# Kernel tuning notes

Hardware: AMD Instinct MI355X
Metric: run time of the kernel (lower is better)

## Reference

```python
import jax, jax.numpy as jnp
import numpy as np

B, S, HID = 4, 1024, 2048
H, D = 16, 128
CACHE_LEN = 2048


def setup_inputs() -> dict:
    key = jax.random.key(0)
    ks = jax.random.split(key, 5)
    return {
        "x": jax.random.normal(ks[0], (B, S, HID), jnp.float32),
        "cached_k": jax.random.normal(ks[1], (CACHE_LEN, H, D), jnp.float32),
        "cached_v": jax.random.normal(ks[2], (CACHE_LEN, H, D), jnp.float32),
        "w_qkv": jax.random.normal(ks[3], (3 * HID, HID), jnp.float32) * 0.02,
        "b_qkv": jnp.zeros((3 * HID,), jnp.float32),
        "w_proj": jax.random.normal(ks[4], (HID, HID), jnp.float32) * 0.02,
        "b_proj": jnp.zeros((HID,), jnp.float32),
    }


def reference(x, cached_k, cached_v, w_qkv, b_qkv, w_proj, b_proj):
    b, s, hid = x.shape
    h, d = H, D
    # fused QKV projection (nn.Linear uses y = x @ W.T + b)
    qkv = x @ w_qkv.T + b_qkv                      # [B,S,3*HID]
    q, k, v = jnp.split(qkv, 3, axis=-1)
    q = q.reshape(b, s, h, d).transpose(0, 2, 1, 3)  # [B,H,S,D]
    k = k.reshape(b, s, h, d).transpose(0, 2, 1, 3)
    v = v.reshape(b, s, h, d).transpose(0, 2, 1, 3)
    # cached KV: [cache_len,H,D] -> [H,cache_len,D] -> broadcast over batch
    clen = cached_k.shape[0]
    ck = jnp.broadcast_to(cached_k.transpose(1, 0, 2)[None], (b, h, clen, d))
    cv = jnp.broadcast_to(cached_v.transpose(1, 0, 2)[None], (b, h, clen, d))
    k = jnp.concatenate([ck, k], axis=2)           # [B,H,clen+S,D]
    v = jnp.concatenate([cv, v], axis=2)
    # non-causal scaled dot-product attention
    scale = 1.0 / jnp.sqrt(jnp.asarray(d, x.dtype))
    scores = jnp.einsum('bhqd,bhkd->bhqk', q, k) * scale
    attn = jax.nn.softmax(scores, axis=-1)
    out = jnp.einsum('bhqk,bhkd->bhqd', attn, v)   # [B,H,S,D]
    out = out.transpose(0, 2, 1, 3).reshape(b, s, hid)
    return out @ w_proj.T + b_proj
```

## Files before the change

### kernel.cpp

```cpp
#include <hip/hip_runtime.h>
#include <cstdint>
#include <cstddef>

typedef _Float16 f16;
typedef _Float16 f16x4 __attribute__((ext_vector_type(4)));
typedef _Float16 f16x8 __attribute__((ext_vector_type(8)));
typedef float f32x4 __attribute__((ext_vector_type(4)));

__device__ __forceinline__ void gld_lds16(const void* gp, void* lp) {
  __builtin_amdgcn_global_load_lds(
      (__attribute__((address_space(1))) void*)(void*)gp,
      (__attribute__((address_space(3))) void*)lp, 16, 0, 0);
}

__global__ __launch_bounds__(256) void cast_plain(const float* __restrict__ in,
                                                  f16* __restrict__ out, int n4) {
  int i = blockIdx.x * 256 + threadIdx.x;
  if (i >= n4) return;
  float4 v = ((const float4*)in)[i];
  f16x4 o = {(f16)v.x, (f16)v.y, (f16)v.z, (f16)v.w};
  ((f16x4*)out)[i] = o;
}

__global__ __launch_bounds__(256) void cast_ck(const float* __restrict__ in,
                                               f16* __restrict__ out) {
  int i = blockIdx.x * 256 + threadIdx.x;
  int d4 = i & 31, hh = (i >> 5) & 15, l = i >> 9;
  float4 v = ((const float4*)in)[((size_t)l * 16 + hh) * 32 + d4];
  f16x4 o = {(f16)v.x, (f16)v.y, (f16)v.z, (f16)v.w};
  ((f16x4*)out)[((size_t)hh * 2048 + l) * 32 + d4] = o;
}

__global__ __launch_bounds__(256) void cast_cvt(const float* __restrict__ in,
                                                f16* __restrict__ out) {
  __shared__ float tl[32][129];
  int hh = blockIdx.x & 15;
  int l0 = (blockIdx.x >> 4) * 32;
  int t = threadIdx.x;
#pragma unroll
  for (int j = 0; j < 4; j++) {
    int idx = j * 256 + t;
    int l = idx >> 5, d4 = idx & 31;
    float4 v = ((const float4*)in)[(((size_t)(l0 + l)) * 16 + hh) * 32 + d4];
    tl[l][d4 * 4 + 0] = v.x;
    tl[l][d4 * 4 + 1] = v.y;
    tl[l][d4 * 4 + 2] = v.z;
    tl[l][d4 * 4 + 3] = v.w;
  }
  __syncthreads();
#pragma unroll
  for (int j = 0; j < 4; j++) {
    int idx = j * 256 + t;
    int d = idx >> 3, l4 = (idx & 7) * 4;
    f16x4 o = {(f16)tl[l4 + 0][d], (f16)tl[l4 + 1][d],
               (f16)tl[l4 + 2][d], (f16)tl[l4 + 3][d]};
    ((f16x4*)(out + ((size_t)hh * 128 + d) * 2048 + l0))[l4 >> 2] = o;
  }
}

template <int EPI>
__global__ __launch_bounds__(256, 2) void gemm_bt(
    const f16* __restrict__ A, const f16* __restrict__ Bm,
    const float* __restrict__ bias, float* __restrict__ Cf, int M, int N, int K,
    f16* __restrict__ qb, f16* __restrict__ knb, f16* __restrict__ vtnb) {
  __shared__ f16 Al[128 * 32];
  __shared__ f16 Bl[128 * 32];
  const int t = threadIdx.x;
  const int lane = t & 63;
  const int w = t >> 6;
  const int bm = blockIdx.x * 128;
  const int bn = blockIdx.y * 128;
  const int wr = w >> 1, wc = w & 1;

  f32x4 acc[4][4] = {};

  const int srow = lane >> 2;
  const int soff = (lane & 3) * 8;
  const int colr = lane & 15;
  const int k0 = (lane >> 4) * 8;

  const int nk = K >> 5;
  for (int kt = 0; kt < nk; kt++) {
#pragma unroll
    for (int j = 0; j < 2; j++) {
      int c = j * 4 + w;
      int r = c * 16 + srow;
      gld_lds16(A + (size_t)(bm + r) * K + (size_t)kt * 32 + soff,
                (char*)Al + c * 1024);
      gld_lds16(Bm + (size_t)(bn + r) * K + (size_t)kt * 32 + soff,
                (char*)Bl + c * 1024);
    }
    __syncthreads();
    f16x8 af[4], bg[4];
#pragma unroll
    for (int mi = 0; mi < 4; mi++)
      af[mi] = *(const f16x8*)&Al[(wr * 64 + mi * 16 + colr) * 32 + k0];
#pragma unroll
    for (int ni = 0; ni < 4; ni++)
      bg[ni] = *(const f16x8*)&Bl[(wc * 64 + ni * 16 + colr) * 32 + k0];
#pragma unroll
    for (int mi = 0; mi < 4; mi++)
#pragma unroll
      for (int ni = 0; ni < 4; ni++)
        acc[mi][ni] = __builtin_amdgcn_mfma_f32_16x16x32_f16(
            af[mi], bg[ni], acc[mi][ni], 0, 0, 0);
    __syncthreads();
  }

  const float scale = 0.08838834764831845f;
#pragma unroll
  for (int mi = 0; mi < 4; mi++) {
#pragma unroll
    for (int ni = 0; ni < 4; ni++) {
      int n = bn + wc * 64 + ni * 16 + colr;
      int m0 = bm + wr * 64 + mi * 16 + ((lane >> 4) << 2);
      float bv = bias[n];
      f32x4 v = acc[mi][ni];
#pragma unroll
      for (int j = 0; j < 4; j++) {
        int m = m0 + j;
        float val = v[j] + bv;
        if (EPI == 0) {
          int bb = m >> 10, s = m & 1023;
          if (n < 2048) {
            int hh = n >> 7, d = n & 127;
            qb[(((size_t)(bb * 16 + hh)) * 1024 + s) * 128 + d] =
                (f16)(val * scale);
          } else if (n < 4096) {
            int n2 = n - 2048, hh = n2 >> 7, d = n2 & 127;
            knb[(((size_t)(bb * 16 + hh)) * 1024 + s) * 128 + d] = (f16)val;
          } else {
            int n2 = n - 4096, hh = n2 >> 7, d = n2 & 127;
            vtnb[((size_t)(bb * 16 + hh) * 128 + d) * 1024 + s] = (f16)val;
          }
        } else {
          Cf[(size_t)m * N + n] = val;
        }
      }
    }
  }
}

__global__ __launch_bounds__(256, 2) void attn_fwd(
    const f16* __restrict__ qb, const f16* __restrict__ knb,
    const f16* __restrict__ vtnb, const f16* __restrict__ ckb,
    const f16* __restrict__ cvtb, f16* __restrict__ attb) {
  __shared__ f16 Kl[64 * 128];
  __shared__ f16 Vl[128 * 64];
  __shared__ f16 Pl[4][32 * 64];
  const int t = threadIdx.x;
  const int lane = t & 63;
  const int w = t >> 6;
  const int qblk = blockIdx.x;
  const int bh = blockIdx.y;
  const int hh = bh & 15;
  const int colr = lane & 15;
  const int k0 = (lane >> 4) * 8;
  const int qbase = qblk * 128 + w * 32;

  f16x8 qf[2][4];
#pragma unroll
  for (int mi = 0; mi < 2; mi++) {
    const f16* Qp = qb + ((size_t)bh * 1024 + qbase + mi * 16 + colr) * 128 + k0;
#pragma unroll
    for (int c = 0; c < 4; c++) qf[mi][c] = *(const f16x8*)(Qp + c * 32);
  }

  float lrun[2][4];
  f32x4 o[2][8];
#pragma unroll
  for (int mi = 0; mi < 2; mi++) {
#pragma unroll
    for (int j = 0; j < 4; j++) lrun[mi][j] = 0.f;
#pragma unroll
    for (int dt = 0; dt < 8; dt++) o[mi][dt] = {0.f, 0.f, 0.f, 0.f};
  }

  const int srowK = lane >> 4;
  const int soffK = (lane & 15) * 8;
  const int srowV = lane >> 3;
  const int soffV = (lane & 7) * 8;
  f16* pw = &Pl[w][0];

  for (int kt = 0; kt < 48; kt++) {
    const int l0 = kt * 64;
    const f16* ks;
    const f16* vs;
    int vstride;
    if (l0 < 2048) {
      ks = ckb + ((size_t)hh * 2048 + l0) * 128;
      vs = cvtb + (size_t)hh * 128 * 2048 + l0;
      vstride = 2048;
    } else {
      ks = knb + ((size_t)bh * 1024 + (l0 - 2048)) * 128;
      vs = vtnb + (size_t)bh * 128 * 1024 + (l0 - 2048);
      vstride = 1024;
    }
#pragma unroll
    for (int j = 0; j < 4; j++) {
      int c = j * 4 + w;
      gld_lds16(ks + (size_t)(c * 4 + srowK) * 128 + soffK, (char*)Kl + c * 1024);
      gld_lds16(vs + (size_t)(c * 8 + srowV) * (size_t)vstride + soffV,
                (char*)Vl + c * 1024);
    }
    __syncthreads();

    f32x4 sc[2][4];
#pragma unroll
    for (int ct = 0; ct < 4; ct++) {
      f16x8 kf[4];
#pragma unroll
      for (int c = 0; c < 4; c++)
        kf[c] = *(const f16x8*)&Kl[(ct * 16 + colr) * 128 + c * 32 + k0];
#pragma unroll
      for (int mi = 0; mi < 2; mi++) {
        f32x4 a = {0.f, 0.f, 0.f, 0.f};
#pragma unroll
        for (int c = 0; c < 4; c++)
          a = __builtin_amdgcn_mfma_f32_16x16x32_f16(qf[mi][c], kf[c], a, 0, 0, 0);
        sc[mi][ct] = a;
      }
    }

#pragma unroll
    for (int mi = 0; mi < 2; mi++) {
#pragma unroll
      for (int j = 0; j < 4; j++) {
        int r = (lane >> 4) * 4 + j;
        float acc = 0.f;
#pragma unroll
        for (int ct = 0; ct < 4; ct++) {
          float p = __expf(sc[mi][ct][j]);
          acc += p;
          pw[(mi * 16 + r) * 64 + ct * 16 + colr] = (f16)p;
        }
        lrun[mi][j] += acc;
      }
    }

    f16x8 pa[2][2];
#pragma unroll
    for (int mi = 0; mi < 2; mi++)
#pragma unroll
      for (int ksl = 0; ksl < 2; ksl++)
        pa[mi][ksl] = *(const f16x8*)&pw[(mi * 16 + colr) * 64 + ksl * 32 + k0];
#pragma unroll
    for (int dt = 0; dt < 8; dt++) {
      f16x8 vf0 = *(const f16x8*)&Vl[(dt * 16 + colr) * 64 + k0];
      f16x8 vf1 = *(const f16x8*)&Vl[(dt * 16 + colr) * 64 + 32 + k0];
#pragma unroll
      for (int mi = 0; mi < 2; mi++) {
        o[mi][dt] = __builtin_amdgcn_mfma_f32_16x16x32_f16(pa[mi][0], vf0,
                                                           o[mi][dt], 0, 0, 0);
        o[mi][dt] = __builtin_amdgcn_mfma_f32_16x16x32_f16(pa[mi][1], vf1,
                                                           o[mi][dt], 0, 0, 0);
      }
    }
    __syncthreads();
  }

  const int bb = bh >> 4;
#pragma unroll
  for (int mi = 0; mi < 2; mi++) {
    float rinv[4];
#pragma unroll
    for (int j = 0; j < 4; j++) {
      float s = lrun[mi][j];
#pragma unroll
      for (int sh = 1; sh < 16; sh <<= 1) s += __shfl_xor(s, sh, 64);
      rinv[j] = 1.0f / s;
    }
#pragma unroll
    for (int dt = 0; dt < 8; dt++) {
#pragma unroll
      for (int j = 0; j < 4; j++) {
        int r = (lane >> 4) * 4 + j;
        int m = bb * 1024 + qblk * 128 + w * 32 + mi * 16 + r;
        int n = hh * 128 + dt * 16 + colr;
        attb[(size_t)m * 2048 + n] = (f16)(o[mi][dt][j] * rinv[j]);
      }
    }
  }
}

extern "C" void kernel_launch(void* const* d_in, const int* in_sizes, int n_in,
                              void* d_out, int out_size, void* d_ws,
                              size_t ws_size, hipStream_t stream) {
  const float* x = (const float*)d_in[0];
  const float* ck = (const float*)d_in[1];
  const float* cv = (const float*)d_in[2];
  const float* wqkv = (const float*)d_in[3];
  const float* bqkv = (const float*)d_in[4];
  const float* wproj = (const float*)d_in[5];
  const float* bproj = (const float*)d_in[6];
  float* out = (float*)d_out;

  char* ws = (char*)d_ws;
  size_t off = 0;
  auto alloc = [&](size_t bytes) {
    char* p = ws + off;
    off += bytes;
    return p;
  };
  f16* xb = (f16*)alloc(4096ull * 2048 * 2);
  f16* wqb = (f16*)alloc(6144ull * 2048 * 2);
  f16* wpb = (f16*)alloc(2048ull * 2048 * 2);
  f16* ckb = (f16*)alloc(16ull * 2048 * 128 * 2);
  f16* cvtb = (f16*)alloc(16ull * 128 * 2048 * 2);
  f16* qb = (f16*)alloc(64ull * 1024 * 128 * 2);
  f16* knb = (f16*)alloc(64ull * 1024 * 128 * 2);
  f16* vtnb = (f16*)alloc(64ull * 128 * 1024 * 2);
  f16* attb = xb;
  (void)ws_size;

  cast_plain<<<8192, 256, 0, stream>>>(x, xb, 2097152);
  cast_plain<<<12288, 256, 0, stream>>>(wqkv, wqb, 3145728);
  cast_plain<<<4096, 256, 0, stream>>>(wproj, wpb, 1048576);
  cast_ck<<<4096, 256, 0, stream>>>(ck, ckb);
  cast_cvt<<<1024, 256, 0, stream>>>(cv, cvtb);

  gemm_bt<0><<<dim3(32, 48), 256, 0, stream>>>(xb, wqb, bqkv, nullptr, 4096,
                                               6144, 2048, qb, knb, vtnb);
  attn_fwd<<<dim3(8, 64), 256, 0, stream>>>(qb, knb, vtnb, ckb, cvtb, attb);
  gemm_bt<1><<<dim3(32, 16), 256, 0, stream>>>(attb, wpb, bproj, out, 4096,
                                               2048, 2048, nullptr, nullptr,
                                               nullptr);
}
```

Baseline: 542.1 us.

## Double-buffer LDS tiles in GEMM and attention, XOR-swizzle attention LDS

Both the projection GEMM and the attention kernel now use two LDS buffers. The next K/V (or A/B) tile is issued with global_load_lds while MFMAs run on the current tile, which hides global load latency behind compute. The attention kernel also XOR-swizzles K, V and the per-wave P tile on both the write and read side to remove LDS bank conflicts caused by the power-of-two row strides. The cost is higher LDS use: attention goes to about 80KB per block, which may limit occupancy to two blocks per CU.

```diff
diff --git a/kernel.cpp b/kernel.cpp
--- a/kernel.cpp
+++ b/kernel.cpp
@@ -1,6 +1,7 @@
 #include <hip/hip_runtime.h>
 #include <cstdint>
 #include <cstddef>
+#include <type_traits>
 
 typedef _Float16 f16;
 typedef _Float16 f16x4 __attribute__((ext_vector_type(4)));
@@ -63,8 +64,8 @@
     const f16* __restrict__ A, const f16* __restrict__ Bm,
     const float* __restrict__ bias, float* __restrict__ Cf, int M, int N, int K,
     f16* __restrict__ qb, f16* __restrict__ knb, f16* __restrict__ vtnb) {
-  __shared__ f16 Al[128 * 32];
-  __shared__ f16 Bl[128 * 32];
+  __shared__ f16 Al[2][128 * 32];
+  __shared__ f16 Bl[2][128 * 32];
   const int t = threadIdx.x;
   const int lane = t & 63;
   const int w = t >> 6;
@@ -78,32 +79,47 @@
   const int soff = (lane & 3) * 8;
   const int colr = lane & 15;
   const int k0 = (lane >> 4) * 8;
-
   const int nk = K >> 5;
-  for (int kt = 0; kt < nk; kt++) {
+
+  auto stage = [&](int kt, auto bufc) {
+    constexpr int buf = decltype(bufc)::value;
 #pragma unroll
     for (int j = 0; j < 2; j++) {
       int c = j * 4 + w;
       int r = c * 16 + srow;
       gld_lds16(A + (size_t)(bm + r) * K + (size_t)kt * 32 + soff,
-                (char*)Al + c * 1024);
+                (char*)&Al[buf][0] + c * 1024);
       gld_lds16(Bm + (size_t)(bn + r) * K + (size_t)kt * 32 + soff,
-                (char*)Bl + c * 1024);
-    }
-    __syncthreads();
+                (char*)&Bl[buf][0] + c * 1024);
+    }
+  };
+  auto tile = [&](auto bufc) {
+    constexpr int buf = decltype(bufc)::value;
     f16x8 af[4], bg[4];
 #pragma unroll
     for (int mi = 0; mi < 4; mi++)
-      af[mi] = *(const f16x8*)&Al[(wr * 64 + mi * 16 + colr) * 32 + k0];
+      af[mi] = *(const f16x8*)&Al[buf][(wr * 64 + mi * 16 + colr) * 32 + k0];
 #pragma unroll
     for (int ni = 0; ni < 4; ni++)
-      bg[ni] = *(const f16x8*)&Bl[(wc * 64 + ni * 16 + colr) * 32 + k0];
+      bg[ni] = *(const f16x8*)&Bl[buf][(wc * 64 + ni * 16 + colr) * 32 + k0];
 #pragma unroll
     for (int mi = 0; mi < 4; mi++)
 #pragma unroll
       for (int ni = 0; ni < 4; ni++)
         acc[mi][ni] = __builtin_amdgcn_mfma_f32_16x16x32_f16(
             af[mi], bg[ni], acc[mi][ni], 0, 0, 0);
+  };
+  std::integral_constant<int, 0> B0;
+  std::integral_constant<int, 1> B1;
+
+  stage(0, B0);
+  __syncthreads();
+  for (int kt = 0; kt < nk; kt += 2) {
+    stage(kt + 1, B1);
+    tile(B0);
+    __syncthreads();
+    if (kt + 2 < nk) stage(kt + 2, B0);
+    tile(B1);
     __syncthreads();
   }
 
@@ -145,8 +161,8 @@
     const f16* __restrict__ qb, const f16* __restrict__ knb,
     const f16* __restrict__ vtnb, const f16* __restrict__ ckb,
     const f16* __restrict__ cvtb, f16* __restrict__ attb) {
-  __shared__ f16 Kl[64 * 128];
-  __shared__ f16 Vl[128 * 64];
+  __shared__ f16 Kl[2][64 * 128];
+  __shared__ f16 Vl[2][128 * 64];
   __shared__ f16 Pl[4][32 * 64];
   const int t = threadIdx.x;
   const int lane = t & 63;
@@ -155,7 +171,8 @@
   const int bh = blockIdx.y;
   const int hh = bh & 15;
   const int colr = lane & 15;
-  const int k0 = (lane >> 4) * 8;
+  const int g = lane >> 4;
+  const int k0 = g * 8;
   const int qbase = qblk * 128 + w * 32;
 
   f16x8 qf[2][4];
@@ -176,13 +193,12 @@
     for (int dt = 0; dt < 8; dt++) o[mi][dt] = {0.f, 0.f, 0.f, 0.f};
   }
 
-  const int srowK = lane >> 4;
-  const int soffK = (lane & 15) * 8;
-  const int srowV = lane >> 3;
-  const int soffV = (lane & 7) * 8;
+  const int csK_l = lane & 15;
+  const int csV_l = lane & 7;
   f16* pw = &Pl[w][0];
 
-  for (int kt = 0; kt < 48; kt++) {
+  auto stage = [&](int kt, auto bufc) {
+    constexpr int buf = decltype(bufc)::value;
     const int l0 = kt * 64;
     const f16* ks;
     const f16* vs;
@@ -199,19 +215,25 @@
 #pragma unroll
     for (int j = 0; j < 4; j++) {
       int c = j * 4 + w;
-      gld_lds16(ks + (size_t)(c * 4 + srowK) * 128 + soffK, (char*)Kl + c * 1024);
-      gld_lds16(vs + (size_t)(c * 8 + srowV) * (size_t)vstride + soffV,
-                (char*)Vl + c * 1024);
-    }
-    __syncthreads();
-
+      int rowK = c * 4 + g;
+      gld_lds16(ks + (size_t)rowK * 128 + ((csK_l ^ (rowK & 7)) * 8),
+                (char*)&Kl[buf][0] + c * 1024);
+      int rowV = c * 8 + (lane >> 3);
+      gld_lds16(vs + (size_t)rowV * (size_t)vstride + ((csV_l ^ (rowV & 7)) * 8),
+                (char*)&Vl[buf][0] + c * 1024);
+    }
+  };
+
+  auto tile = [&](auto bufc) {
+    constexpr int buf = decltype(bufc)::value;
     f32x4 sc[2][4];
 #pragma unroll
     for (int ct = 0; ct < 4; ct++) {
       f16x8 kf[4];
 #pragma unroll
       for (int c = 0; c < 4; c++)
-        kf[c] = *(const f16x8*)&Kl[(ct * 16 + colr) * 128 + c * 32 + k0];
+        kf[c] = *(const f16x8*)&Kl[buf][(ct * 16 + colr) * 128 +
+                                        ((c * 32 + k0) ^ ((colr & 7) << 3))];
 #pragma unroll
       for (int mi = 0; mi < 2; mi++) {
         f32x4 a = {0.f, 0.f, 0.f, 0.f};
@@ -226,28 +248,33 @@
     for (int mi = 0; mi < 2; mi++) {
 #pragma unroll
       for (int j = 0; j < 4; j++) {
-        int r = (lane >> 4) * 4 + j;
-        float acc = 0.f;
+        int rowp = mi * 16 + g * 4 + j;
+        float acc2 = 0.f;
 #pragma unroll
         for (int ct = 0; ct < 4; ct++) {
           float p = __expf(sc[mi][ct][j]);
-          acc += p;
-          pw[(mi * 16 + r) * 64 + ct * 16 + colr] = (f16)p;
+          acc2 += p;
+          pw[rowp * 64 + ((ct ^ g) * 16) + colr] = (f16)p;
         }
-        lrun[mi][j] += acc;
+        lrun[mi][j] += acc2;
       }
     }
 
     f16x8 pa[2][2];
 #pragma unroll
-    for (int mi = 0; mi < 2; mi++)
+    for (int mi = 0; mi < 2; mi++) {
+      int rowp = mi * 16 + colr;
+      int sp = ((colr >> 2) & 3) << 4;
 #pragma unroll
       for (int ksl = 0; ksl < 2; ksl++)
-        pa[mi][ksl] = *(const f16x8*)&pw[(mi * 16 + colr) * 64 + ksl * 32 + k0];
+        pa[mi][ksl] = *(const f16x8*)&pw[rowp * 64 + ((ksl * 32 + k0) ^ sp)];
+    }
+    const int sv = (colr & 7) << 3;
 #pragma unroll
     for (int dt = 0; dt < 8; dt++) {
-      f16x8 vf0 = *(const f16x8*)&Vl[(dt * 16 + colr) * 64 + k0];
-      f16x8 vf1 = *(const f16x8*)&Vl[(dt * 16 + colr) * 64 + 32 + k0];
+      int rowv = dt * 16 + colr;
+      f16x8 vf0 = *(const f16x8*)&Vl[buf][rowv * 64 + (k0 ^ sv)];
+      f16x8 vf1 = *(const f16x8*)&Vl[buf][rowv * 64 + ((32 + k0) ^ sv)];
 #pragma unroll
       for (int mi = 0; mi < 2; mi++) {
         o[mi][dt] = __builtin_amdgcn_mfma_f32_16x16x32_f16(pa[mi][0], vf0,
@@ -256,6 +283,19 @@
                                                            o[mi][dt], 0, 0, 0);
       }
     }
+  };
+
+  std::integral_constant<int, 0> B0;
+  std::integral_constant<int, 1> B1;
+
+  stage(0, B0);
+  __syncthreads();
+  for (int kt = 0; kt < 48; kt += 2) {
+    stage(kt + 1, B1);
+    tile(B0);
+    __syncthreads();
+    if (kt + 2 < 48) stage(kt + 2, B0);
+    tile(B1);
     __syncthreads();
   }
 
@@ -274,7 +314,7 @@
     for (int dt = 0; dt < 8; dt++) {
 #pragma unroll
       for (int j = 0; j < 4; j++) {
-        int r = (lane >> 4) * 4 + j;
+        int r = g * 4 + j;
         int m = bb * 1024 + qblk * 128 + w * 32 + mi * 16 + r;
         int n = hh * 128 + dt * 16 + colr;
         attb[(size_t)m * 2048 + n] = (f16)(o[mi][dt][j] * rinv[j]);
```

Result: faster. 500.0 us (-7.8%).
